# Optimization experiments

Hardware: AMD Instinct MI355X
Metric: run time of the kernel (lower is better)

## Reference

```python
import jax, jax.numpy as jnp
import numpy as np

N_TV_ITER = 20      # fixed Chambolle iteration count (skimage early-stops via eps; fixed for jit)
TV_WEIGHT = 0.1


def _div(p):
    # negative adjoint of forward-difference gradient (skimage convention)
    d = -(p[0] + p[1])
    d = d.at[1:, :].add(p[0, :-1, :])
    d = d.at[:, 1:].add(p[1, :, :-1])
    return d


def tv_chambolle_2d(image):
    """skimage.restoration.denoise_tv_chambolle on a single 2D image, weight=0.1."""
    tau = 0.25  # 1 / (2 * ndim)

    def step(p, _):
        out = image + _div(p)
        gy = jnp.zeros_like(out).at[:-1, :].set(out[1:, :] - out[:-1, :])
        gx = jnp.zeros_like(out).at[:, :-1].set(out[:, 1:] - out[:, :-1])
        norm = jnp.sqrt(gy * gy + gx * gx)
        g = jnp.stack([gy, gx])
        p = (p - tau * g) / (1.0 + (tau / TV_WEIGHT) * norm)
        return p, None

    p0 = jnp.zeros((2,) + image.shape, image.dtype)
    p, _ = jax.lax.scan(step, p0, None, length=N_TV_ITER)
    return image + _div(p)


def tv_denoise(img):  # [B,C,H,W], vmapped over B*C (replaces the CPU python loop)
    B, C, H, W = img.shape
    out = jax.vmap(tv_chambolle_2d)(img.reshape(B * C, H, W))
    return out.reshape(B, C, H, W)


def conv(x, w, stride=1, groups=1):
    pad = w.shape[2] // 2  # 'same'-style padding for odd kernels, 0 for 1x1
    return jax.lax.conv_general_dilated(
        x, w, (stride, stride), [(pad, pad), (pad, pad)],
        dimension_numbers=('NCHW', 'OIHW', 'NCHW'),
        feature_group_count=groups)


def haar_ll(x):
    # one level of pywt wavedec2('haar') LL band: 0.5 * sum over each 2x2 block
    return 0.5 * (x[..., ::2, ::2] + x[..., ::2, 1::2] + x[..., 1::2, ::2] + x[..., 1::2, 1::2])


def backbone(x, stem_w, dw_pw):
    # stride-32, 1280-channel EfficientNet-B0-style feature extractor
    x = jax.nn.silu(conv(x, stem_w, stride=2))
    for dw, pw in dw_pw:
        x = jax.nn.silu(conv(x, dw, stride=2, groups=dw.shape[0]))
        x = jax.nn.silu(conv(x, pw))
    return x


def setup_inputs() -> dict:
    key = jax.random.key(0)
    ks = jax.random.split(key, 16)
    B, H, W = 4, 512, 512

    def w(k, o, i, kh, kw):
        return jax.random.normal(k, (o, i, kh, kw), jnp.float32) * (1.0 / np.sqrt(i * kh * kw))

    return {
        "img": jax.random.normal(ks[0], (B, 1, H, W), jnp.float32),
        "stem_w": w(ks[1], 32, 1, 3, 3),
        "dw1_w": w(ks[2], 32, 1, 3, 3),  "pw1_w": w(ks[3], 64, 32, 1, 1),
        "dw2_w": w(ks[4], 64, 1, 3, 3),  "pw2_w": w(ks[5], 128, 64, 1, 1),
        "dw3_w": w(ks[6], 128, 1, 3, 3), "pw3_w": w(ks[7], 256, 128, 1, 1),
        "dw4_w": w(ks[8], 256, 1, 3, 3), "pw4_w": w(ks[9], 512, 256, 1, 1),
        "head_w": w(ks[10], 1280, 512, 1, 1),
        "proj_w": w(ks[11], 64, 1280, 1, 1),
        "proj_b": jnp.zeros((64,), jnp.float32),
        "final_w": w(ks[12], 1, 64, 1, 1),
        "final_b": jnp.zeros((1,), jnp.float32),
    }


def reference(img, stem_w, dw1_w, pw1_w, dw2_w, pw2_w, dw3_w, pw3_w, dw4_w, pw4_w,
              head_w, proj_w, proj_b, final_w, final_b):
    B, C, H, W = img.shape
    x = tv_denoise(img)                                     # fused TV Chambolle
    x = backbone(x, stem_w, [(dw1_w, pw1_w), (dw2_w, pw2_w), (dw3_w, pw3_w), (dw4_w, pw4_w)])
    x = jax.nn.silu(conv(x, head_w))                        # [B,1280,H/32,W/32]
    x = conv(x, proj_w) + proj_b[None, :, None, None]       # [B,64,H/32,W/32]
    x = jax.image.resize(x, (B, 64, H, W), method='bilinear')  # align_corners=False semantics
    ll = haar_ll(haar_ll(x))                                # 2-level Haar LL: [B,64,H/4,W/4]
    out = conv(ll, final_w) + final_b[None, :, None, None]  # [B,1,H/4,W/4]
    return out
```

## Files before the change

### kernel.cpp

```cpp
#include <hip/hip_runtime.h>
#include <math.h>

constexpr int BATCH = 4;
constexpr int IMG_H = 512, IMG_W = 512;
constexpr int IMG_HW = IMG_H * IMG_W;
constexpr int PSTR = BATCH * IMG_HW;

constexpr size_t O_PA   = 0;
constexpr size_t O_PB   = O_PA + 2 * (size_t)PSTR;
constexpr size_t O_DEN  = O_PB + 2 * (size_t)PSTR;
constexpr size_t O_A1   = O_DEN + (size_t)PSTR;
constexpr size_t O_A2   = O_A1 + 8388608;
constexpr size_t O_WT1  = O_A2 + 2097152;
constexpr size_t O_WT2  = O_WT1 + 32 * 64;
constexpr size_t O_WT3  = O_WT2 + 64 * 128;
constexpr size_t O_WT4  = O_WT3 + 128 * 256;
constexpr size_t O_WTH  = O_WT4 + 256 * 512;
constexpr size_t O_WCOMB= O_WTH + 512 * 1280;
constexpr size_t O_BCOMB= O_WCOMB + 1280;
constexpr size_t O_S    = O_BCOMB + 4;
constexpr size_t WS_FLOATS = O_S + 1024;

__device__ __forceinline__ float fast_rcp(float x) { return __builtin_amdgcn_rcpf(x); }
__device__ __forceinline__ float fast_sqrt(float x) { return __builtin_amdgcn_sqrtf(x); }
__device__ __forceinline__ float silu_f(float x) {
    float e = __builtin_amdgcn_exp2f(-1.44269504088896f * x);
    return x * fast_rcp(1.0f + e);
}
__device__ __forceinline__ int clampi(int v, int lo, int hi) {
    return v < lo ? lo : (v > hi ? hi : v);
}

template <int NST, bool FIRST, bool LAST>
__global__ __launch_bounds__(512, 8) void tv_reg(const float* __restrict__ img,
                                                 const float* __restrict__ pin,
                                                 float* __restrict__ pout,
                                                 const float* __restrict__ pw1,
                                                 const float* __restrict__ pw2,
                                                 const float* __restrict__ pw3,
                                                 const float* __restrict__ pw4,
                                                 const float* __restrict__ headw,
                                                 const float* __restrict__ projw,
                                                 const float* __restrict__ projb,
                                                 const float* __restrict__ finalw,
                                                 float* __restrict__ ws) {
    constexpr int ROWS = 6, NW = 8, HL = 10, TC = 44, TR = 28;
    constexpr int TVY = 19;
    __shared__ float bndP[2][512], bndO[2][512];

    if constexpr (FIRST) {
        if (blockIdx.y >= TVY) {
            __shared__ float tt[32][33];
            const int tid = threadIdx.x;
            const int pid = ((blockIdx.y - TVY) * 4 + blockIdx.z) * 12 + blockIdx.x;
            for (int t = pid; t < 814; t += 96) {
                const float* src = nullptr; float* dst = nullptr;
                int C = 0, R = 0, tr = 0, tc = 0;
                if (t < 640) {
                    src = headw; dst = ws + O_WTH; R = 1280; C = 512; tr = t >> 4; tc = t & 15;
                } else if (t < 768) {
                    int e = t - 640; src = pw4; dst = ws + O_WT4; R = 512; C = 256; tr = e >> 3; tc = e & 7;
                } else if (t < 800) {
                    int e = t - 768; src = pw3; dst = ws + O_WT3; R = 256; C = 128; tr = e >> 2; tc = e & 3;
                } else if (t < 808) {
                    int e = t - 800; src = pw2; dst = ws + O_WT2; R = 128; C = 64; tr = e >> 1; tc = e & 1;
                } else if (t < 810) {
                    int e = t - 808; src = pw1; dst = ws + O_WT1; R = 64; C = 32; tr = e; tc = 0;
                }
                const int tx = tid & 31, ty = tid >> 5;
                __syncthreads();
                if (src) {
#pragma unroll
                    for (int j = 0; j < 2; ++j)
                        tt[ty + j * 16][tx] =
                            src[(size_t)(tr * 32 + ty + j * 16) * C + tc * 32 + tx];
                }
                __syncthreads();
                if (src) {
#pragma unroll
                    for (int j = 0; j < 2; ++j)
                        dst[(size_t)(tc * 32 + ty + j * 16) * R + tr * 32 + tx] =
                            tt[tx][ty + j * 16];
                } else if (t < 813) {
                    int k = (t - 810) * 512 + tid;
                    if (k < 1280) {
                        float a = 0.0f;
                        for (int ch = 0; ch < 64; ++ch)
                            a = fmaf(finalw[ch], projw[ch * 1280 + k], a);
                        ws[O_WCOMB + k] = a;
                    }
                } else {
                    if (tid == 0) {
                        float a = 0.0f;
                        for (int ch = 0; ch < 64; ++ch) a = fmaf(finalw[ch], projb[ch], a);
                        ws[O_BCOMB] = a;
                    }
                }
            }
            return;
        }
    }

    const int tid = threadIdx.x;
    const int lane = tid & 63, w = tid >> 6;
    const int b = blockIdx.z;
    const int r0 = blockIdx.y * TR, c0 = blockIdx.x * TC;
    const int gj = c0 - HL + lane;
    const int gjc = clampi(gj, 0, 511);
    const int gib = r0 - HL + w * ROWS;
    const float* I = img + b * IMG_HW;
    const bool interior = (r0 - HL >= 1) && (r0 + NW * ROWS - HL <= 511) &&
                          (c0 - HL >= 1) && (c0 + 64 - HL <= 511);

    float rim[ROWS], rp0[ROWS], rp1[ROWS], ro[ROWS];
#pragma unroll
    for (int k = 0; k < ROWS; ++k) {
        int gi = clampi(gib + k, 0, 511);
        rim[k] = I[(gi << 9) + gjc];
    }
    if (!FIRST) {
        const float* P0 = pin + b * IMG_HW;
        const float* P1 = pin + PSTR + b * IMG_HW;
#pragma unroll
        for (int k = 0; k < ROWS; ++k) {
            int gi = clampi(gib + k, 0, 511);
            rp0[k] = P0[(gi << 9) + gjc];
            rp1[k] = P1[(gi << 9) + gjc];
        }
    }
    const bool gjpos = (gj > 0), gjlt = (gj < 511);

    int s0 = 0;
    if (FIRST) {
        bndO[0][tid] = rim[0];
        __syncthreads();
        float odn = (w < NW - 1) ? bndO[0][tid + 64] : 0.0f;
        if (interior) {
#pragma unroll
            for (int k = 0; k < ROWS; ++k) {
                float oR = __shfl_down(rim[k], 1);
                float od = (k < ROWS - 1) ? rim[k + 1] : odn;
                float gy = od - rim[k];
                float gx = oR - rim[k];
                float inv = fast_rcp(fmaf(2.5f, fast_sqrt(fmaf(gy, gy, gx * gx)), 1.0f));
                rp0[k] = -0.25f * gy * inv;
                rp1[k] = -0.25f * gx * inv;
            }
        } else {
#pragma unroll
            for (int k = 0; k < ROWS; ++k) {
                float oR = __shfl_down(rim[k], 1);
                float od = (k < ROWS - 1) ? rim[k + 1] : odn;
                int gi = gib + k;
                float gy = (gi < 511) ? od - rim[k] : 0.0f;
                float gx = gjlt ? oR - rim[k] : 0.0f;
                float inv = fast_rcp(fmaf(2.5f, fast_sqrt(fmaf(gy, gy, gx * gx)), 1.0f));
                rp0[k] = -0.25f * gy * inv;
                rp1[k] = -0.25f * gx * inv;
            }
        }
        s0 = 1;
    }

    for (int s = s0; s < NST; ++s) {
        const int par = s & 1;
        float p1l0 = __shfl_up(rp1[0], 1);
        float partO = rim[0] - rp0[0] - rp1[0];
        if (interior) partO += p1l0;
        else if (gjpos) partO += p1l0;
        bndP[par][tid] = rp0[ROWS - 1];
        bndO[par][tid] = partO;
        __syncthreads();
        float pup0 = (w > 0) ? bndP[par][tid - 64] : 0.0f;
        float odn = (w < NW - 1) ? bndO[par][tid + 64] + rp0[ROWS - 1] : 0.0f;
        if (interior) {
            ro[0] = partO + pup0;
#pragma unroll
            for (int k = 1; k < ROWS; ++k) {
                float p1l = __shfl_up(rp1[k], 1);
                ro[k] = rim[k] - rp0[k] - rp1[k] + rp0[k - 1] + p1l;
            }
#pragma unroll
            for (int k = 0; k < ROWS; ++k) {
                float oR = __shfl_down(ro[k], 1);
                float od = (k < ROWS - 1) ? ro[k + 1] : odn;
                float gy = od - ro[k];
                float gx = oR - ro[k];
                float inv = fast_rcp(fmaf(2.5f, fast_sqrt(fmaf(gy, gy, gx * gx)), 1.0f));
                rp0[k] = (rp0[k] - 0.25f * gy) * inv;
                rp1[k] = (rp1[k] - 0.25f * gx) * inv;
            }
        } else {
            ro[0] = partO + ((gib > 0) ? pup0 : 0.0f);
#pragma unroll
            for (int k = 1; k < ROWS; ++k) {
                float p1l = __shfl_up(rp1[k], 1);
                float o = rim[k] - rp0[k] - rp1[k];
                if (gib + k > 0) o += rp0[k - 1];
                if (gjpos) o += p1l;
                ro[k] = o;
            }
#pragma unroll
            for (int k = 0; k < ROWS; ++k) {
                float oR = __shfl_down(ro[k], 1);
                float od = (k < ROWS - 1) ? ro[k + 1] : odn;
                int gi = gib + k;
                float gy = (gi < 511) ? od - ro[k] : 0.0f;
                float gx = gjlt ? oR - ro[k] : 0.0f;
                float inv = fast_rcp(fmaf(2.5f, fast_sqrt(fmaf(gy, gy, gx * gx)), 1.0f));
                rp0[k] = (rp0[k] - 0.25f * gy) * inv;
                rp1[k] = (rp1[k] - 0.25f * gx) * inv;
            }
        }
    }

    const bool cst = (lane >= HL && lane < HL + TC && gj < 512);
    if (LAST) {
        constexpr int epar = NST & 1;
        bndP[epar][tid] = rp0[ROWS - 1];
        __syncthreads();
        float pup0 = (w > 0) ? bndP[epar][tid - 64] : 0.0f;
        float* D = pout + b * IMG_HW;
#pragma unroll
        for (int k = 0; k < ROWS; ++k) {
            float p1l = __shfl_up(rp1[k], 1);
            int gi = gib + k;
            int rk = w * ROWS + k;
            float o = rim[k] - rp0[k] - rp1[k];
            float pup = (k > 0) ? rp0[k - 1] : pup0;
            if (gi > 0) o += pup;
            if (gjpos) o += p1l;
            if (rk >= HL && rk < HL + TR && cst && gi < 512) D[(gi << 9) + gj] = o;
        }
    } else {
        float* Q0 = pout + b * IMG_HW;
        float* Q1 = pout + PSTR + b * IMG_HW;
#pragma unroll
        for (int k = 0; k < ROWS; ++k) {
            int rk = w * ROWS + k;
            int gi = gib + k;
            if (rk >= HL && rk < HL + TR && cst && gi < 512) {
                Q0[(gi << 9) + gj] = rp0[k];
                Q1[(gi << 9) + gj] = rp1[k];
            }
        }
    }
}

__global__ __launch_bounds__(256) void stem_dw1_pw1(const float* __restrict__ den,
                                                    const float* __restrict__ stemw,
                                                    const float* __restrict__ dw1w,
                                                    const float* __restrict__ pw1T,
                                                    float* __restrict__ out) {
    __shared__ float sDen[35 * 36];
    __shared__ float sStem[8 * 323];
    __shared__ float sDw[32 * 64];
    __shared__ float sW[576];
    __shared__ __align__(16) float sWp[2048];
    const int tid = threadIdx.x;
    const int b = blockIdx.z;
    const int r0 = blockIdx.y * 32, c0 = blockIdx.x * 32;
    const float* D = den + b * IMG_HW;
    for (int e = tid; e < 576; e += 256) sW[e] = (e < 288) ? stemw[e] : dw1w[e - 288];
    for (int e = tid; e < 2048; e += 256) sWp[e] = pw1T[e];
    for (int e = tid; e < 35 * 35; e += 256) {
        int li = e / 35, lj = e % 35;
        int gi = r0 - 3 + li, gjj = c0 - 3 + lj;
        sDen[li * 36 + lj] = (gi >= 0 && gjj >= 0) ? D[(gi << 9) + gjj] : 0.0f;
    }
    __syncthreads();

    for (int g = 0; g < 4; ++g) {
        if (g) __syncthreads();
        for (int e = tid; e < 2312; e += 256) {
            int pos = e >> 3, cl = e & 7;
            int sy = pos / 17, sx = pos % 17;
            int c = 8 * g + cl;
            const float* wc = &sW[c * 9];
            const float* dbase = &sDen[(2 * sy) * 36 + 2 * sx];
            float a = 0.0f;
#pragma unroll
            for (int ky = 0; ky < 3; ++ky)
#pragma unroll
                for (int kx = 0; kx < 3; ++kx)
                    a = fmaf(wc[ky * 3 + kx], dbase[ky * 36 + kx], a);
            sStem[cl * 323 + sy * 19 + sx] = silu_f(a);
        }
        __syncthreads();
        for (int e = tid; e < 512; e += 256) {
            int cl = e >> 6, dy = (e >> 3) & 7, dx = e & 7;
            int c = 8 * g + cl;
            float acc = 0.0f;
#pragma unroll
            for (int ky = 0; ky < 3; ++ky)
#pragma unroll
                for (int kx = 0; kx < 3; ++kx) {
                    int sgy = (r0 >> 1) - 1 + 2 * dy + ky;
                    int sgx = (c0 >> 1) - 1 + 2 * dx + kx;
                    float v = (sgy >= 0 && sgx >= 0)
                        ? sStem[cl * 323 + (2 * dy + ky) * 19 + 2 * dx + kx] : 0.0f;
                    acc = fmaf(sW[288 + c * 9 + ky * 3 + kx], v, acc);
                }
            sDw[c * 64 + (dy << 3) + dx] = silu_f(acc);
        }
    }
    __syncthreads();

    const int px = tid & 63, oc0 = (tid >> 6) * 16;
    float acc[16];
#pragma unroll
    for (int j = 0; j < 16; ++j) acc[j] = 0.0f;
    for (int ic = 0; ic < 32; ++ic) {
        float v = sDw[ic * 64 + px];
        const float* wr = &sWp[ic * 64 + oc0];
#pragma unroll
        for (int q = 0; q < 4; ++q) {
            float4 w4 = *(const float4*)(wr + q * 4);
            acc[q * 4 + 0] = fmaf(v, w4.x, acc[q * 4 + 0]);
            acc[q * 4 + 1] = fmaf(v, w4.y, acc[q * 4 + 1]);
            acc[q * 4 + 2] = fmaf(v, w4.z, acc[q * 4 + 2]);
            acc[q * 4 + 3] = fmaf(v, w4.w, acc[q * 4 + 3]);
        }
    }
    const int gpos = ((r0 >> 2) + (px >> 3)) * 128 + (c0 >> 2) + (px & 7);
    float* ob = out + (size_t)b * 64 * 16384 + (size_t)oc0 * 16384 + gpos;
#pragma unroll
    for (int j = 0; j < 16; ++j) ob[(size_t)j * 16384] = silu_f(acc[j]);
}

template <int C, int HIN>
__global__ __launch_bounds__(256) void dw_kernel(const float* __restrict__ in,
                                                 const float* __restrict__ w,
                                                 float* __restrict__ out) {
    constexpr int HO = HIN / 2;
    int t = blockIdx.x * 256 + threadIdx.x;
    int x = t % HO;
    int y = (t / HO) % HO;
    int c = (t / (HO * HO)) % C;
    int b = t / (HO * HO * C);
    const float* I = in + ((size_t)(b * C + c)) * (HIN * HIN);
    const float* wc = w + c * 9;
    int iy = 2 * y - 1, ix = 2 * x - 1;
    float acc = 0.0f;
#pragma unroll
    for (int ky = 0; ky < 3; ++ky)
#pragma unroll
        for (int kx = 0; kx < 3; ++kx) {
            int yy = iy + ky, xx = ix + kx;
            float vv = (yy >= 0 && xx >= 0) ? I[yy * HIN + xx] : 0.0f;
            acc = fmaf(wc[ky * 3 + kx], vv, acc);
        }
    out[t] = silu_f(acc);
}

template <int C, int HIN>
__global__ __launch_bounds__(256) void dw_reduce2_kernel(const float* __restrict__ part,
                                                         const float* __restrict__ w,
                                                         float* __restrict__ out) {
    constexpr int HO = HIN / 2;
    int t = blockIdx.x * 256 + threadIdx.x;
    int x = t % HO;
    int y = (t / HO) % HO;
    int c = (t / (HO * HO)) % C;
    int b = t / (HO * HO * C);
    const float* Ia = part + ((size_t)(b * C + c)) * (HIN * HIN);
    const float* Ib = Ia + (size_t)BATCH * C * HIN * HIN;
    const float* wc = w + c * 9;
    int iy = 2 * y - 1, ix = 2 * x - 1;
    float acc = 0.0f;
#pragma unroll
    for (int ky = 0; ky < 3; ++ky)
#pragma unroll
        for (int kx = 0; kx < 3; ++kx) {
            int yy = iy + ky, xx = ix + kx;
            float vv = 0.0f;
            if (yy >= 0 && xx >= 0) {
                int o = yy * HIN + xx;
                vv = silu_f(Ia[o] + Ib[o]);
            }
            acc = fmaf(wc[ky * 3 + kx], vv, acc);
        }
    out[t] = silu_f(acc);
}

template <int ICT, int NSIN, int NSPLIT, int OC, bool SILU>
__global__ __launch_bounds__(256) void pw_gemm(const float* __restrict__ in,
                                               const float* __restrict__ wT,
                                               float* __restrict__ out,
                                               int HW) {
    constexpr int KC = 32, TP = 64, TOC = 64, OPT = 4, PPT = 4;
    constexpr int KS = ICT / NSPLIT;
    constexpr int NC = KS / KC;
    constexpr int NOG = TOC / OPT;
    constexpr int PV4 = KC * TP / 4 / 256;
    constexpr int WV4 = KC * TOC / 4 / 256;
    static_assert(KS % KC == 0, "split");
    __shared__ __align__(16) float sPx[2][KC * TP];
    __shared__ __align__(16) float sW[2][KC * TOC];
    const int tid = threadIdx.x;
    const int zb = blockIdx.z;
    const int b = zb / NSPLIT, ks = zb % NSPLIT;
    const int p0 = blockIdx.x * TP;
    const int oc0 = blockIdx.y * TOC;
    const int ocg = tid % NOG, pxg = tid / NOG;
    const size_t instride = (size_t)BATCH * ICT * HW;
    const float* gin0 = in + ((size_t)b * ICT + ks * KS) * HW + p0;
    const float* gw0  = wT + ((size_t)(ks * KS)) * OC + oc0;

    float4 rp[PV4], rw[WV4];
    auto load_chunk = [&](int cc) {
        const float* gin = gin0 + (size_t)cc * KC * HW;
#pragma unroll
        for (int i = 0; i < PV4; ++i) {
            int e = tid + i * 256;
            int row = e / (TP / 4), col = e % (TP / 4);
            const float* base = gin + (size_t)row * HW + col * 4;
            float4 a = *(const float4*)base;
#pragma unroll
            for (int s = 1; s < NSIN; ++s) {
                float4 t4 = *(const float4*)(base + (size_t)s * instride);
                a.x += t4.x; a.y += t4.y; a.z += t4.z; a.w += t4.w;
            }
            if (NSIN > 1) {
                a.x = silu_f(a.x); a.y = silu_f(a.y);
                a.z = silu_f(a.z); a.w = silu_f(a.w);
            }
            rp[i] = a;
        }
        const float* gw = gw0 + (size_t)cc * KC * OC;
#pragma unroll
        for (int i = 0; i < WV4; ++i) {
            int e = tid + i * 256;
            int row = e / (TOC / 4), col = e % (TOC / 4);
            rw[i] = *(const float4*)(gw + (size_t)row * OC + col * 4);
        }
    };
    auto store_chunk = [&](int buf) {
#pragma unroll
        for (int i = 0; i < PV4; ++i) ((float4*)sPx[buf])[tid + i * 256] = rp[i];
#pragma unroll
        for (int i = 0; i < WV4; ++i) ((float4*)sW[buf])[tid + i * 256] = rw[i];
    };

    float acc[OPT][PPT];
#pragma unroll
    for (int o = 0; o < OPT; ++o)
#pragma unroll
        for (int p = 0; p < PPT; ++p) acc[o][p] = 0.0f;

    load_chunk(0);
    store_chunk(0);
    __syncthreads();
    for (int cc = 0; cc < NC; ++cc) {
        if (cc + 1 < NC) load_chunk(cc + 1);
        const int buf = cc & 1;
#pragma unroll 4
        for (int k = 0; k < KC; ++k) {
            float4 pv = *(const float4*)&sPx[buf][k * TP + pxg * PPT];
            float4 wv = *(const float4*)&sW[buf][k * TOC + ocg * OPT];
            float w0 = wv.x, w1 = wv.y, w2 = wv.z, w3 = wv.w;
            acc[0][0] = fmaf(pv.x, w0, acc[0][0]);
            acc[0][1] = fmaf(pv.y, w0, acc[0][1]);
            acc[0][2] = fmaf(pv.z, w0, acc[0][2]);
            acc[0][3] = fmaf(pv.w, w0, acc[0][3]);
            acc[1][0] = fmaf(pv.x, w1, acc[1][0]);
            acc[1][1] = fmaf(pv.y, w1, acc[1][1]);
            acc[1][2] = fmaf(pv.z, w1, acc[1][2]);
            acc[1][3] = fmaf(pv.w, w1, acc[1][3]);
            acc[2][0] = fmaf(pv.x, w2, acc[2][0]);
            acc[2][1] = fmaf(pv.y, w2, acc[2][1]);
            acc[2][2] = fmaf(pv.z, w2, acc[2][2]);
            acc[2][3] = fmaf(pv.w, w2, acc[2][3]);
            acc[3][0] = fmaf(pv.x, w3, acc[3][0]);
            acc[3][1] = fmaf(pv.y, w3, acc[3][1]);
            acc[3][2] = fmaf(pv.z, w3, acc[3][2]);
            acc[3][3] = fmaf(pv.w, w3, acc[3][3]);
        }
        if (cc + 1 < NC) {
            store_chunk((cc + 1) & 1);
            __syncthreads();
        }
    }

    float* ob;
    if (NSPLIT == 1)
        ob = out + ((size_t)(b * OC + oc0 + ocg * OPT)) * HW + p0 + pxg * PPT;
    else
        ob = out + (((size_t)(ks * BATCH + b)) * OC + oc0 + ocg * OPT) * HW + p0 + pxg * PPT;
#pragma unroll
    for (int o = 0; o < OPT; ++o) {
        float4 r;
        r.x = SILU ? silu_f(acc[o][0]) : acc[o][0];
        r.y = SILU ? silu_f(acc[o][1]) : acc[o][1];
        r.z = SILU ? silu_f(acc[o][2]) : acc[o][2];
        r.w = SILU ? silu_f(acc[o][3]) : acc[o][3];
        *(float4*)(ob + (size_t)o * HW) = r;
    }
}

__global__ __launch_bounds__(512) void head_fused(const float* __restrict__ in,
                                                  const float* __restrict__ wT,
                                                  const float* __restrict__ wcomb,
                                                  float* __restrict__ partial) {
    constexpr int ICT = 512, KC = 32, TP = 32, TOC = 64, OC = 1280, HW = 256;
    constexpr int NCG = 8;
    __shared__ __align__(16) float smem[4096 + 8192 + 512];
    float* pxBuf = smem;
    float* wBuf  = smem + 4096;
    float* dotred= smem + 12288;
    float* kred  = smem;
    const int tid = threadIdx.x;
    const int g = tid >> 8, lt = tid & 255;
    const int b = blockIdx.z;
    const int p0 = blockIdx.x * TP;
    const int oc0 = blockIdx.y * TOC;
    const int ocg = lt & 15, pxg = lt >> 4;
    const size_t instride = (size_t)BATCH * ICT * HW;
    const float* gin0 = in + (size_t)b * ICT * HW + p0;

    float4 rp, rw[2];
    auto load_chunk = [&](int cc) {
        const float* gin = gin0 + (size_t)(g * NCG + cc) * KC * HW;
        {
            int row = lt >> 3, col = lt & 7;
            const float* base = gin + (size_t)row * HW + col * 4;
            float4 a = *(const float4*)base;
#pragma unroll
            for (int s = 1; s < 4; ++s) {
                float4 t4 = *(const float4*)(base + (size_t)s * instride);
                a.x += t4.x; a.y += t4.y; a.z += t4.z; a.w += t4.w;
            }
            a.x = silu_f(a.x); a.y = silu_f(a.y);
            a.z = silu_f(a.z); a.w = silu_f(a.w);
            rp = a;
        }
        const float* gw = wT + (size_t)(g * NCG + cc) * KC * OC + oc0;
#pragma unroll
        for (int i = 0; i < 2; ++i) {
            int e = lt + i * 256;
            int row = e >> 4, col = e & 15;
            rw[i] = *(const float4*)(gw + (size_t)row * OC + col * 4);
        }
    };
    auto store_chunk = [&](int buf) {
        ((float4*)(pxBuf + (g * 2 + buf) * 1024))[lt] = rp;
#pragma unroll
        for (int i = 0; i < 2; ++i)
            ((float4*)(wBuf + (g * 2 + buf) * 2048))[lt + i * 256] = rw[i];
    };

    float acc[4][2];
#pragma unroll
    for (int o = 0; o < 4; ++o) { acc[o][0] = 0.0f; acc[o][1] = 0.0f; }

    load_chunk(0);
    store_chunk(0);
    __syncthreads();
    for (int cc = 0; cc < NCG; ++cc) {
        if (cc + 1 < NCG) load_chunk(cc + 1);
        const float* sp = pxBuf + (g * 2 + (cc & 1)) * 1024;
        const float* sw = wBuf + (g * 2 + (cc & 1)) * 2048;
#pragma unroll 4
        for (int k = 0; k < KC; ++k) {
            float2 pv = *(const float2*)&sp[k * TP + pxg * 2];
            float4 wv = *(const float4*)&sw[k * TOC + ocg * 4];
            acc[0][0] = fmaf(pv.x, wv.x, acc[0][0]);
            acc[0][1] = fmaf(pv.y, wv.x, acc[0][1]);
            acc[1][0] = fmaf(pv.x, wv.y, acc[1][0]);
            acc[1][1] = fmaf(pv.y, wv.y, acc[1][1]);
            acc[2][0] = fmaf(pv.x, wv.z, acc[2][0]);
            acc[2][1] = fmaf(pv.y, wv.z, acc[2][1]);
            acc[3][0] = fmaf(pv.x, wv.w, acc[3][0]);
            acc[3][1] = fmaf(pv.y, wv.w, acc[3][1]);
        }
        if (cc + 1 < NCG) {
            store_chunk((cc + 1) & 1);
            __syncthreads();
        }
    }

    __syncthreads();
    if (g == 1) {
#pragma unroll
        for (int o = 0; o < 4; ++o) {
            kred[lt * 8 + o * 2 + 0] = acc[o][0];
            kred[lt * 8 + o * 2 + 1] = acc[o][1];
        }
    }
    __syncthreads();
    if (g == 0) {
#pragma unroll
        for (int o = 0; o < 4; ++o) {
            acc[o][0] += kred[lt * 8 + o * 2 + 0];
            acc[o][1] += kred[lt * 8 + o * 2 + 1];
        }
        float4 wc4 = *(const float4*)(wcomb + oc0 + ocg * 4);
#pragma unroll
        for (int p = 0; p < 2; ++p) {
            float v = wc4.x * silu_f(acc[0][p]);
            v = fmaf(wc4.y, silu_f(acc[1][p]), v);
            v = fmaf(wc4.z, silu_f(acc[2][p]), v);
            v = fmaf(wc4.w, silu_f(acc[3][p]), v);
            dotred[(pxg * 2 + p) * 16 + ocg] = v;
        }
    }
    __syncthreads();
    if (tid < 32) {
        float a = 0.0f;
#pragma unroll
        for (int gg = 0; gg < 16; ++gg) a += dotred[tid * 16 + gg];
        partial[((size_t)blockIdx.y * 4 + b) * 256 + p0 + tid] = a;
    }
}

__global__ __launch_bounds__(256) void resize_haar(const float* __restrict__ partial,
                                                   const float* __restrict__ bcomb,
                                                   const float* __restrict__ finalb,
                                                   float* __restrict__ out) {
    __shared__ float sS[256];
    int t = blockIdx.x * 256 + threadIdx.x;
    int c = t & 127, r = (t >> 7) & 127, b = t >> 14;
    {
        float a = bcomb[0];
        const float* P = partial + (size_t)b * 256 + threadIdx.x;
        for (int y = 0; y < 20; ++y) a += P[(size_t)y * 1024];
        sS[threadIdx.x] = a;
    }
    __syncthreads();
    const float* S = sS;
    float acc = 0.0f;
#pragma unroll
    for (int j = 0; j < 4; ++j) {
        float sy = ((4 * r + j) + 0.5f) * (1.0f / 32.0f) - 0.5f;
        int y0 = (int)floorf(sy);
        float fy = sy - (float)y0;
        int ya = y0 < 0 ? 0 : y0;
        int yb = (y0 + 1) > 15 ? 15 : (y0 + 1);
#pragma unroll
        for (int i = 0; i < 4; ++i) {
            float sx = ((4 * c + i) + 0.5f) * (1.0f / 32.0f) - 0.5f;
            int x0 = (int)floorf(sx);
            float fx = sx - (float)x0;
            int xa = x0 < 0 ? 0 : x0;
            int xb = (x0 + 1) > 15 ? 15 : (x0 + 1);
            float v0 = S[ya * 16 + xa] * (1.0f - fx) + S[ya * 16 + xb] * fx;
            float v1 = S[yb * 16 + xa] * (1.0f - fx) + S[yb * 16 + xb] * fx;
            acc += v0 * (1.0f - fy) + v1 * fy;
        }
    }
    out[t] = 0.25f * acc + finalb[0];
}

extern "C" void kernel_launch(void* const* d_in, const int* in_sizes, int n_in,
                              void* d_out, int out_size, void* d_ws, size_t ws_size,
                              hipStream_t stream) {
    if (ws_size < WS_FLOATS * sizeof(float)) return;

    const float* img    = (const float*)d_in[0];
    const float* stem_w = (const float*)d_in[1];
    const float* dw1_w  = (const float*)d_in[2];
    const float* pw1_w  = (const float*)d_in[3];
    const float* dw2_w  = (const float*)d_in[4];
    const float* pw2_w  = (const float*)d_in[5];
    const float* dw3_w  = (const float*)d_in[6];
    const float* pw3_w  = (const float*)d_in[7];
    const float* dw4_w  = (const float*)d_in[8];
    const float* pw4_w  = (const float*)d_in[9];
    const float* head_w = (const float*)d_in[10];
    const float* proj_w = (const float*)d_in[11];
    const float* proj_b = (const float*)d_in[12];
    const float* final_w= (const float*)d_in[13];
    const float* final_b= (const float*)d_in[14];
    float* ws  = (float*)d_ws;
    float* out = (float*)d_out;

    dim3 tvg1(12, 21, 4), tvg2(12, 19, 4);
    tv_reg<10, true,  false><<<tvg1, 512, 0, stream>>>(
        img, img, ws + O_PA,
        pw1_w, pw2_w, pw3_w, pw4_w, head_w, proj_w, proj_b, final_w, ws);
    tv_reg<10, false, true ><<<tvg2, 512, 0, stream>>>(
        img, ws + O_PA, ws + O_DEN,
        nullptr, nullptr, nullptr, nullptr, nullptr, nullptr, nullptr, nullptr, ws);

    stem_dw1_pw1<<<dim3(16, 16, 4), 256, 0, stream>>>(ws + O_DEN, stem_w, dw1_w,
                                                      ws + O_WT1, ws + O_A1);

    dw_kernel<64, 128><<<4096, 256, 0, stream>>>(ws + O_A1, dw2_w, ws + O_A2);
    pw_gemm<64, 1, 2, 128, false><<<dim3(64, 2, 8), 256, 0, stream>>>(ws + O_A2, ws + O_WT2, ws + O_PA, 4096);

    dw_reduce2_kernel<128, 64><<<2048, 256, 0, stream>>>(ws + O_PA, dw3_w, ws + O_A1);
    pw_gemm<128, 1, 2, 256, false><<<dim3(16, 4, 8), 256, 0, stream>>>(ws + O_A1, ws + O_WT3, ws + O_PA, 1024);

    dw_reduce2_kernel<256, 32><<<1024, 256, 0, stream>>>(ws + O_PA, dw4_w, ws + O_A2);
    pw_gemm<256, 1, 4, 512, false><<<dim3(4, 8, 16), 256, 0, stream>>>(ws + O_A2, ws + O_WT4, ws + O_PA, 256);

    head_fused<<<dim3(8, 20, 4), 512, 0, stream>>>(ws + O_PA, ws + O_WTH, ws + O_WCOMB, ws + O_A1);

    resize_haar<<<256, 256, 0, stream>>>(ws + O_A1, ws + O_BCOMB, final_b, out);
}
```

Before: 242.9 us.

## Split-K presum+SiLU into separate kernel and double pixel tile in head GEMM

Moves the sum of the four split-K partials and the SiLU out of the head GEMM's load path into a small standalone kernel. Previously every output-channel block redid that work. The head GEMM then loads the activated input directly and widens the pixel tile from 32 to 64, giving each thread a 4x4 accumulator instead of 4x2. That halves the number of blocks and raises compute per shared-memory load. The cost is an extra launch and one extra global round trip, plus more shared memory and registers per block.

```diff
diff --git a/kernel.cpp b/kernel.cpp
--- a/kernel.cpp
+++ b/kernel.cpp
@@ -498,16 +498,32 @@
     }
 }
 
-__global__ __launch_bounds__(512) void head_fused(const float* __restrict__ in,
+__global__ __launch_bounds__(256) void presum_silu(const float* __restrict__ part,
+                                                   float* __restrict__ xout) {
+    constexpr size_t PS = (size_t)BATCH * 512 * 256;
+    int t = blockIdx.x * 256 + threadIdx.x;
+    const float* p = part + (size_t)t * 4;
+    float4 a = *(const float4*)p;
+    float4 b = *(const float4*)(p + PS);
+    float4 c = *(const float4*)(p + 2 * PS);
+    float4 d = *(const float4*)(p + 3 * PS);
+    a.x += b.x; a.y += b.y; a.z += b.z; a.w += b.w;
+    a.x += c.x; a.y += c.y; a.z += c.z; a.w += c.w;
+    a.x += d.x; a.y += d.y; a.z += d.z; a.w += d.w;
+    a.x = silu_f(a.x); a.y = silu_f(a.y); a.z = silu_f(a.z); a.w = silu_f(a.w);
+    *(float4*)(xout + (size_t)t * 4) = a;
+}
+
+__global__ __launch_bounds__(512) void head_fused(const float* __restrict__ x,
                                                   const float* __restrict__ wT,
                                                   const float* __restrict__ wcomb,
                                                   float* __restrict__ partial) {
-    constexpr int ICT = 512, KC = 32, TP = 32, TOC = 64, OC = 1280, HW = 256;
+    constexpr int KC = 32, TP = 64, TOC = 64, OC = 1280, HW = 256;
     constexpr int NCG = 8;
-    __shared__ __align__(16) float smem[4096 + 8192 + 512];
+    __shared__ __align__(16) float smem[8192 + 8192 + 1024];
     float* pxBuf = smem;
-    float* wBuf  = smem + 4096;
-    float* dotred= smem + 12288;
+    float* wBuf  = smem + 8192;
+    float* dotred= smem + 16384;
     float* kred  = smem;
     const int tid = threadIdx.x;
     const int g = tid >> 8, lt = tid & 255;
@@ -515,24 +531,16 @@
     const int p0 = blockIdx.x * TP;
     const int oc0 = blockIdx.y * TOC;
     const int ocg = lt & 15, pxg = lt >> 4;
-    const size_t instride = (size_t)BATCH * ICT * HW;
-    const float* gin0 = in + (size_t)b * ICT * HW + p0;
-
-    float4 rp, rw[2];
+    const float* gin0 = x + (size_t)b * 512 * HW + p0;
+
+    float4 rp[2], rw[2];
     auto load_chunk = [&](int cc) {
         const float* gin = gin0 + (size_t)(g * NCG + cc) * KC * HW;
-        {
-            int row = lt >> 3, col = lt & 7;
-            const float* base = gin + (size_t)row * HW + col * 4;
-            float4 a = *(const float4*)base;
-#pragma unroll
-            for (int s = 1; s < 4; ++s) {
-                float4 t4 = *(const float4*)(base + (size_t)s * instride);
-                a.x += t4.x; a.y += t4.y; a.z += t4.z; a.w += t4.w;
-            }
-            a.x = silu_f(a.x); a.y = silu_f(a.y);
-            a.z = silu_f(a.z); a.w = silu_f(a.w);
-            rp = a;
+#pragma unroll
+        for (int i = 0; i < 2; ++i) {
+            int e = lt + i * 256;
+            int row = e >> 4, col = e & 15;
+            rp[i] = *(const float4*)(gin + (size_t)row * HW + col * 4);
         }
         const float* gw = wT + (size_t)(g * NCG + cc) * KC * OC + oc0;
 #pragma unroll
@@ -543,35 +551,46 @@
         }
     };
     auto store_chunk = [&](int buf) {
-        ((float4*)(pxBuf + (g * 2 + buf) * 1024))[lt] = rp;
-#pragma unroll
-        for (int i = 0; i < 2; ++i)
-            ((float4*)(wBuf + (g * 2 + buf) * 2048))[lt + i * 256] = rw[i];
+#pragma unroll
+        for (int i = 0; i < 2; ++i) {
+            ((float4*)(pxBuf + (g * 2 + buf) * 2048))[lt + i * 256] = rp[i];
+            ((float4*)(wBuf  + (g * 2 + buf) * 2048))[lt + i * 256] = rw[i];
+        }
     };
 
-    float acc[4][2];
-#pragma unroll
-    for (int o = 0; o < 4; ++o) { acc[o][0] = 0.0f; acc[o][1] = 0.0f; }
+    float acc[4][4];
+#pragma unroll
+    for (int o = 0; o < 4; ++o)
+#pragma unroll
+        for (int p = 0; p < 4; ++p) acc[o][p] = 0.0f;
 
     load_chunk(0);
     store_chunk(0);
     __syncthreads();
     for (int cc = 0; cc < NCG; ++cc) {
         if (cc + 1 < NCG) load_chunk(cc + 1);
-        const float* sp = pxBuf + (g * 2 + (cc & 1)) * 1024;
+        const float* sp = pxBuf + (g * 2 + (cc & 1)) * 2048;
         const float* sw = wBuf + (g * 2 + (cc & 1)) * 2048;
-#pragma unroll 4
+#pragma unroll 2
         for (int k = 0; k < KC; ++k) {
-            float2 pv = *(const float2*)&sp[k * TP + pxg * 2];
+            float4 pv = *(const float4*)&sp[k * TP + pxg * 4];
             float4 wv = *(const float4*)&sw[k * TOC + ocg * 4];
             acc[0][0] = fmaf(pv.x, wv.x, acc[0][0]);
             acc[0][1] = fmaf(pv.y, wv.x, acc[0][1]);
+            acc[0][2] = fmaf(pv.z, wv.x, acc[0][2]);
+            acc[0][3] = fmaf(pv.w, wv.x, acc[0][3]);
             acc[1][0] = fmaf(pv.x, wv.y, acc[1][0]);
             acc[1][1] = fmaf(pv.y, wv.y, acc[1][1]);
+            acc[1][2] = fmaf(pv.z, wv.y, acc[1][2]);
+            acc[1][3] = fmaf(pv.w, wv.y, acc[1][3]);
             acc[2][0] = fmaf(pv.x, wv.z, acc[2][0]);
             acc[2][1] = fmaf(pv.y, wv.z, acc[2][1]);
+            acc[2][2] = fmaf(pv.z, wv.z, acc[2][2]);
+            acc[2][3] = fmaf(pv.w, wv.z, acc[2][3]);
             acc[3][0] = fmaf(pv.x, wv.w, acc[3][0]);
             acc[3][1] = fmaf(pv.y, wv.w, acc[3][1]);
+            acc[3][2] = fmaf(pv.z, wv.w, acc[3][2]);
+            acc[3][3] = fmaf(pv.w, wv.w, acc[3][3]);
         }
         if (cc + 1 < NCG) {
             store_chunk((cc + 1) & 1);
@@ -582,30 +601,28 @@
     __syncthreads();
     if (g == 1) {
 #pragma unroll
-        for (int o = 0; o < 4; ++o) {
-            kred[lt * 8 + o * 2 + 0] = acc[o][0];
-            kred[lt * 8 + o * 2 + 1] = acc[o][1];
-        }
+        for (int o = 0; o < 4; ++o)
+#pragma unroll
+            for (int p = 0; p < 4; ++p) kred[lt * 16 + o * 4 + p] = acc[o][p];
     }
     __syncthreads();
     if (g == 0) {
 #pragma unroll
-        for (int o = 0; o < 4; ++o) {
-            acc[o][0] += kred[lt * 8 + o * 2 + 0];
-            acc[o][1] += kred[lt * 8 + o * 2 + 1];
-        }
+        for (int o = 0; o < 4; ++o)
+#pragma unroll
+            for (int p = 0; p < 4; ++p) acc[o][p] += kred[lt * 16 + o * 4 + p];
         float4 wc4 = *(const float4*)(wcomb + oc0 + ocg * 4);
 #pragma unroll
-        for (int p = 0; p < 2; ++p) {
+        for (int p = 0; p < 4; ++p) {
             float v = wc4.x * silu_f(acc[0][p]);
             v = fmaf(wc4.y, silu_f(acc[1][p]), v);
             v = fmaf(wc4.z, silu_f(acc[2][p]), v);
             v = fmaf(wc4.w, silu_f(acc[3][p]), v);
-            dotred[(pxg * 2 + p) * 16 + ocg] = v;
+            dotred[(pxg * 4 + p) * 16 + ocg] = v;
         }
     }
     __syncthreads();
-    if (tid < 32) {
+    if (tid < 64) {
         float a = 0.0f;
 #pragma unroll
         for (int gg = 0; gg < 16; ++gg) a += dotred[tid * 16 + gg];
@@ -694,7 +711,9 @@
     dw_reduce2_kernel<256, 32><<<1024, 256, 0, stream>>>(ws + O_PA, dw4_w, ws + O_A2);
     pw_gemm<256, 1, 4, 512, false><<<dim3(4, 8, 16), 256, 0, stream>>>(ws + O_A2, ws + O_WT4, ws + O_PA, 256);
 
-    head_fused<<<dim3(8, 20, 4), 512, 0, stream>>>(ws + O_PA, ws + O_WTH, ws + O_WCOMB, ws + O_A1);
+    presum_silu<<<512, 256, 0, stream>>>(ws + O_PA, ws + O_A2);
+
+    head_fused<<<dim3(4, 20, 4), 512, 0, stream>>>(ws + O_A2, ws + O_WTH, ws + O_WCOMB, ws + O_A1);
 
     resize_haar<<<256, 256, 0, stream>>>(ws + O_A1, ws + O_BCOMB, final_b, out);
 }
```

Measured after the change: 244.4 us. About the same (+0.6%).
